# Kernel tuning notes

Hardware: AMD Instinct MI355X
Metric: run time of the kernel (lower is better)

Reference implementation:

```python
import jax, jax.numpy as jnp
import numpy as np

LN_EPS = 1e-5
LEAKY_SLOPE = 0.2


def setup_inputs() -> dict:
    key = jax.random.key(0)
    k = jax.random.split(key, 6)
    B, N, D, H, hd = 32768, 4, 256, 4, 64
    out_dim = H * hd
    # Weights stored as (in_dim, out_dim) so projection is h @ W (same math as torch Linear with W.T)
    return {
        "h": jax.random.normal(k[0], (B, N, D), dtype=jnp.float32),
        "edge_bias": jax.random.normal(k[1], (N, N), dtype=jnp.float32),
        "W_l": jax.random.normal(k[2], (D, out_dim), dtype=jnp.float32) * (1.0 / np.sqrt(D)),
        "W_r": jax.random.normal(k[3], (D, out_dim), dtype=jnp.float32) * (1.0 / np.sqrt(D)),
        "a": jax.random.normal(k[4], (H, hd), dtype=jnp.float32) * (1.0 / np.sqrt(hd)),
        "ln_gamma": jnp.ones((out_dim,), dtype=jnp.float32),
        "ln_beta": jnp.zeros((out_dim,), dtype=jnp.float32),
    }


def reference(h, edge_bias, W_l, W_r, a, ln_gamma, ln_beta):
    B, N, _ = h.shape
    H, d = a.shape
    g_l = (h @ W_l).reshape(B, N, H, d)
    g_r = (h @ W_r).reshape(B, N, H, d)
    # GATv2 dynamic attention: LeakyReLU applied BEFORE scoring with a
    pairwise = jax.nn.leaky_relu(g_l[:, :, None] + g_r[:, None, :], LEAKY_SLOPE)  # (B,N,N,H,d)
    e = jnp.einsum('bijhd,hd->bijh', pairwise, a)  # (B,N,N,H)
    e = e + edge_bias[None, :, :, None]
    alpha = jax.nn.softmax(e, axis=2)  # softmax over neighbor j
    # dropout is identity in eval mode
    h_prime = jnp.einsum('bijh,bjhd->bihd', alpha, g_r).reshape(B, N, H * d)
    # LayerNorm over last dim
    mu = jnp.mean(h_prime, axis=-1, keepdims=True)
    var = jnp.var(h_prime, axis=-1, keepdims=True)
    out = (h_prime - mu) * jax.lax.rsqrt(var + LN_EPS) * ln_gamma + ln_beta
    return out
```

## Files before the change

### kernel.cpp

```cpp
#include <hip/hip_runtime.h>
#include <hip/hip_bf16.h>

typedef short bf16x8 __attribute__((ext_vector_type(8)));
typedef float f32x4 __attribute__((ext_vector_type(4)));

#define LN_EPS 1e-5f
#define SLOPE 0.2f

__device__ __forceinline__ unsigned short f2bf(float f){
  __hip_bfloat16 b = __float2bfloat16(f);
  return *reinterpret_cast<unsigned short*>(&b);
}

__global__ void wconv_kernel(const float* __restrict__ Wl,
                             const float* __restrict__ Wr,
                             unsigned short* __restrict__ wbf){
  int idx = blockIdx.x * 256 + threadIdx.x;
  int c = idx & 511;
  int gg = (idx >> 9) & 3;
  int s = idx >> 11;
  int k0 = s * 32 + gg * 8;
  const float* src = (c < 256) ? (Wl + c) : (Wr + (c - 256));
  bf16x8 v;
  #pragma unroll
  for (int j = 0; j < 8; ++j) v[j] = (short)f2bf(src[(k0 + j) * 256]);
  *(bf16x8*)&wbf[(size_t)idx * 8] = v;
}

template<bool USE_WS>
__global__ __launch_bounds__(256, 2)
void gat_fused(const float* __restrict__ hin, const float* __restrict__ ebias,
               const float* __restrict__ Wl, const float* __restrict__ Wr,
               const float* __restrict__ avec, const float* __restrict__ gmw,
               const float* __restrict__ btw, const unsigned short* __restrict__ wbf,
               float* __restrict__ out){
  __shared__ __align__(16) unsigned short uni[8192];
  __shared__ float red1[128], red2[128];
  __shared__ float eb_s[16];

  const int t = threadIdx.x;
  const int lane = t & 63;
  const int w = t >> 6;
  const int b0 = blockIdx.x * 8;
  const int g = lane >> 4;
  const int ln = lane & 15;

  float av[4];
  #pragma unroll
  for (int c = 0; c < 4; ++c) av[c] = avec[w * 64 + c * 16 + ln];
  if (t < 16) eb_s[t] = ebias[t];

  {
    const float* hb = hin + (size_t)b0 * 1024;
    #pragma unroll
    for (int it = 0; it < 4; ++it){
      int q = it * 256 + t;
      int row = q >> 5;
      int c = q & 31;
      const float* src = hb + row * 256 + c * 8;
      float4 f0 = *(const float4*)src;
      float4 f1 = *(const float4*)(src + 4);
      bf16x8 v;
      v[0]=(short)f2bf(f0.x); v[1]=(short)f2bf(f0.y); v[2]=(short)f2bf(f0.z); v[3]=(short)f2bf(f0.w);
      v[4]=(short)f2bf(f1.x); v[5]=(short)f2bf(f1.y); v[6]=(short)f2bf(f1.z); v[7]=(short)f2bf(f1.w);
      *(bf16x8*)&uni[row * 256 + ((c ^ (row & 7)) << 3)] = v;
    }
  }
  __syncthreads();

  f32x4 acc[2][8];
  #pragma unroll
  for (int m = 0; m < 2; ++m)
    #pragma unroll
    for (int c = 0; c < 8; ++c)
      acc[m][c] = (f32x4){0.f, 0.f, 0.f, 0.f};

  for (int step = 0; step < 8; ++step){
    bf16x8 af[2], bfr[8];
    #pragma unroll
    for (int m = 0; m < 2; ++m){
      int row = m * 16 + ln;
      int chunk = step * 4 + g;
      af[m] = *(const bf16x8*)&uni[row * 256 + ((chunk ^ (row & 7)) << 3)];
    }
    if constexpr (USE_WS){
      const unsigned short* wp = wbf + (size_t)step * 16384 + (size_t)g * 4096
                               + (size_t)(w * 64 + ln) * 8;
      #pragma unroll
      for (int c = 0; c < 4; ++c){
        bfr[c]     = *(const bf16x8*)(wp + c * 128);
        bfr[c + 4] = *(const bf16x8*)(wp + 2048 + c * 128);
      }
    } else {
      #pragma unroll
      for (int c = 0; c < 4; ++c){
        int col = w * 64 + c * 16 + ln;
        #pragma unroll
        for (int j = 0; j < 8; ++j){
          bfr[c][j]     = (short)f2bf(Wl[(step * 32 + g * 8 + j) * 256 + col]);
          bfr[c + 4][j] = (short)f2bf(Wr[(step * 32 + g * 8 + j) * 256 + col]);
        }
      }
    }
    __builtin_amdgcn_s_setprio(1);
    #pragma unroll
    for (int m = 0; m < 2; ++m)
      #pragma unroll
      for (int c = 0; c < 8; ++c)
        acc[m][c] = __builtin_amdgcn_mfma_f32_16x16x32_bf16(af[m], bfr[c], acc[m][c], 0, 0, 0);
    __builtin_amdgcn_s_setprio(0);
  }

  #pragma unroll
  for (int m = 0; m < 2; ++m){
    float e[16];
    #pragma unroll
    for (int q = 0; q < 16; ++q) e[q] = 0.f;
    #pragma unroll
    for (int c = 0; c < 4; ++c){
      f32x4 GL = acc[m][c];
      f32x4 GR = acc[m][c + 4];
      #pragma unroll
      for (int i = 0; i < 4; ++i)
        #pragma unroll
        for (int j = 0; j < 4; ++j){
          float x = GL[i] + GR[j];
          x = fmaxf(x, SLOPE * x);
          e[i * 4 + j] = fmaf(x, av[c], e[i * 4 + j]);
        }
    }
    #pragma unroll
    for (int mask = 1; mask <= 8; mask <<= 1)
      #pragma unroll
      for (int q = 0; q < 16; ++q)
        e[q] += __shfl_xor(e[q], mask);
    #pragma unroll
    for (int q = 0; q < 16; ++q) e[q] += eb_s[q];
    #pragma unroll
    for (int i = 0; i < 4; ++i){
      float mx = fmaxf(fmaxf(e[i*4+0], e[i*4+1]), fmaxf(e[i*4+2], e[i*4+3]));
      float p0 = __expf(e[i*4+0] - mx);
      float p1 = __expf(e[i*4+1] - mx);
      float p2 = __expf(e[i*4+2] - mx);
      float p3 = __expf(e[i*4+3] - mx);
      float rs = 1.f / (p0 + p1 + p2 + p3);
      e[i*4+0] = p0 * rs; e[i*4+1] = p1 * rs; e[i*4+2] = p2 * rs; e[i*4+3] = p3 * rs;
    }
    float hp[4][4];
    #pragma unroll
    for (int i = 0; i < 4; ++i){
      #pragma unroll
      for (int c = 0; c < 4; ++c){
        f32x4 GR = acc[m][c + 4];
        float v = e[i*4+0] * GR[0];
        v = fmaf(e[i*4+1], GR[1], v);
        v = fmaf(e[i*4+2], GR[2], v);
        v = fmaf(e[i*4+3], GR[3], v);
        hp[i][c] = v;
      }
      float s1 = hp[i][0] + hp[i][1] + hp[i][2] + hp[i][3];
      float s2 = fmaf(hp[i][0], hp[i][0],
                 fmaf(hp[i][1], hp[i][1],
                 fmaf(hp[i][2], hp[i][2], hp[i][3] * hp[i][3])));
      #pragma unroll
      for (int mask = 1; mask <= 8; mask <<= 1){
        s1 += __shfl_xor(s1, mask);
        s2 += __shfl_xor(s2, mask);
      }
      int r = (m * 4 + g) * 4 + i;
      if (ln == 0){ red1[r * 4 + w] = s1; red2[r * 4 + w] = s2; }
    }
    __syncthreads();

    float gmr[4], btr[4];
    #pragma unroll
    for (int c = 0; c < 4; ++c){
      gmr[c] = gmw[w * 64 + c * 16 + ln];
      btr[c] = btw[w * 64 + c * 16 + ln];
    }
    #pragma unroll
    for (int i = 0; i < 4; ++i){
      int r = (m * 4 + g) * 4 + i;
      float4 v1 = *(const float4*)&red1[r * 4];
      float4 v2 = *(const float4*)&red2[r * 4];
      float s1 = (v1.x + v1.y) + (v1.z + v1.w);
      float s2 = (v2.x + v2.y) + (v2.z + v2.w);
      float mu = s1 * (1.f / 256.f);
      float var = s2 * (1.f / 256.f) - mu * mu;
      float inv = rsqrtf(var + LN_EPS);
      float* op = out + ((size_t)b0 * 4 + r) * 256 + w * 64 + ln;
      #pragma unroll
      for (int c = 0; c < 4; ++c)
        op[c * 16] = fmaf((hp[i][c] - mu) * inv, gmr[c], btr[c]);
    }
  }
}

extern "C" void kernel_launch(void* const* d_in, const int* in_sizes, int n_in,
                              void* d_out, int out_size, void* d_ws, size_t ws_size,
                              hipStream_t stream){
  const float* h  = (const float*)d_in[0];
  const float* eb = (const float*)d_in[1];
  const float* Wl = (const float*)d_in[2];
  const float* Wr = (const float*)d_in[3];
  const float* a  = (const float*)d_in[4];
  const float* gm = (const float*)d_in[5];
  const float* bt = (const float*)d_in[6];
  float* out = (float*)d_out;
  (void)n_in; (void)out_size;

  int B = in_sizes[0] / 1024;
  int nblk = B / 8;

  if (ws_size >= 262144){
    unsigned short* wbf = (unsigned short*)d_ws;
    wconv_kernel<<<64, 256, 0, stream>>>(Wl, Wr, wbf);
    gat_fused<true><<<nblk, 256, 0, stream>>>(h, eb, Wl, Wr, a, gm, bt, wbf, out);
  } else {
    gat_fused<false><<<nblk, 256, 0, stream>>>(h, eb, Wl, Wr, a, gm, bt, nullptr, out);
  }
}
```

Baseline: 97.06 us.

## Split fused GAT kernel into GEMM and attention kernels via bf16 workspace

Splits the single fused kernel into a projection GEMM kernel that writes g_l/g_r as bf16 into a workspace, and a separate attention+LayerNorm kernel that reads them back. The aim is to lower register pressure and let each phase run at better occupancy. In exchange it adds a global round trip of about 128MB of bf16 intermediates plus an extra launch, and rounds the projection outputs to bf16, which costs precision. The path is taken only when the workspace is large enough.

```diff
diff --git a/kernel.cpp b/kernel.cpp
--- a/kernel.cpp
+++ b/kernel.cpp
@@ -7,6 +7,9 @@
 #define LN_EPS 1e-5f
 #define SLOPE 0.2f
 
+__device__ __forceinline__ float bf2f(unsigned short s){
+  return __uint_as_float(((unsigned)s) << 16);
+}
 __device__ __forceinline__ unsigned short f2bf(float f){
   __hip_bfloat16 b = __float2bfloat16(f);
   return *reinterpret_cast<unsigned short*>(&b);
@@ -25,6 +28,190 @@
   #pragma unroll
   for (int j = 0; j < 8; ++j) v[j] = (short)f2bf(src[(k0 + j) * 256]);
   *(bf16x8*)&wbf[(size_t)idx * 8] = v;
+}
+
+__global__ __launch_bounds__(256, 2)
+void gemm_g(const float* __restrict__ hin, const unsigned short* __restrict__ wbf,
+            unsigned short* __restrict__ gws){
+  __shared__ __align__(16) unsigned short uni[8192];
+  const int t = threadIdx.x;
+  const int lane = t & 63;
+  const int w = t >> 6;
+  const int b0 = blockIdx.x * 8;
+  const int g = lane >> 4;
+  const int ln = lane & 15;
+
+  {
+    const float* hb = hin + (size_t)b0 * 1024;
+    #pragma unroll
+    for (int it = 0; it < 4; ++it){
+      int q = it * 256 + t;
+      int row = q >> 5;
+      int c = q & 31;
+      const float* src = hb + row * 256 + c * 8;
+      float4 f0 = *(const float4*)src;
+      float4 f1 = *(const float4*)(src + 4);
+      bf16x8 v;
+      v[0]=(short)f2bf(f0.x); v[1]=(short)f2bf(f0.y); v[2]=(short)f2bf(f0.z); v[3]=(short)f2bf(f0.w);
+      v[4]=(short)f2bf(f1.x); v[5]=(short)f2bf(f1.y); v[6]=(short)f2bf(f1.z); v[7]=(short)f2bf(f1.w);
+      *(bf16x8*)&uni[row * 256 + ((c ^ (row & 7)) << 3)] = v;
+    }
+  }
+  __syncthreads();
+
+  f32x4 acc[2][8];
+  #pragma unroll
+  for (int m = 0; m < 2; ++m)
+    #pragma unroll
+    for (int c = 0; c < 8; ++c)
+      acc[m][c] = (f32x4){0.f, 0.f, 0.f, 0.f};
+
+  for (int step = 0; step < 8; ++step){
+    bf16x8 af[2], bfr[8];
+    #pragma unroll
+    for (int m = 0; m < 2; ++m){
+      int row = m * 16 + ln;
+      int chunk = step * 4 + g;
+      af[m] = *(const bf16x8*)&uni[row * 256 + ((chunk ^ (row & 7)) << 3)];
+    }
+    const unsigned short* wp = wbf + (size_t)step * 16384 + (size_t)g * 4096
+                             + (size_t)(w * 64 + ln) * 8;
+    #pragma unroll
+    for (int c = 0; c < 4; ++c){
+      bfr[c]     = *(const bf16x8*)(wp + c * 128);
+      bfr[c + 4] = *(const bf16x8*)(wp + 2048 + c * 128);
+    }
+    __builtin_amdgcn_s_setprio(1);
+    #pragma unroll
+    for (int m = 0; m < 2; ++m)
+      #pragma unroll
+      for (int c = 0; c < 8; ++c)
+        acc[m][c] = __builtin_amdgcn_mfma_f32_16x16x32_bf16(af[m], bfr[c], acc[m][c], 0, 0, 0);
+    __builtin_amdgcn_s_setprio(0);
+  }
+
+  #pragma unroll
+  for (int m = 0; m < 2; ++m)
+    #pragma unroll
+    for (int c = 0; c < 8; ++c){
+      ushort4 s;
+      s.x = f2bf(acc[m][c][0]); s.y = f2bf(acc[m][c][1]);
+      s.z = f2bf(acc[m][c][2]); s.w = f2bf(acc[m][c][3]);
+      size_t idx16 = (((size_t)blockIdx.x * 4 + w) * 2 + m) * 8 + c;
+      *(ushort4*)&gws[idx16 * 256 + lane * 4] = s;
+    }
+}
+
+__global__ __launch_bounds__(256, 2)
+void attn_g(const unsigned short* __restrict__ gws, const float* __restrict__ ebias,
+            const float* __restrict__ avec, const float* __restrict__ gmw,
+            const float* __restrict__ btw, float* __restrict__ out){
+  __shared__ float red1[128], red2[128];
+  __shared__ float eb_s[16];
+  const int t = threadIdx.x;
+  const int lane = t & 63;
+  const int w = t >> 6;
+  const int b0 = blockIdx.x * 8;
+  const int g = lane >> 4;
+  const int ln = lane & 15;
+
+  float av[4];
+  #pragma unroll
+  for (int c = 0; c < 4; ++c) av[c] = avec[w * 64 + c * 16 + ln];
+  if (t < 16) eb_s[t] = ebias[t];
+  __syncthreads();
+
+  #pragma unroll
+  for (int m = 0; m < 2; ++m){
+    f32x4 acc[8];
+    #pragma unroll
+    for (int c = 0; c < 8; ++c){
+      size_t idx16 = (((size_t)blockIdx.x * 4 + w) * 2 + m) * 8 + c;
+      ushort4 s = *(const ushort4*)&gws[idx16 * 256 + lane * 4];
+      acc[c] = (f32x4){bf2f(s.x), bf2f(s.y), bf2f(s.z), bf2f(s.w)};
+    }
+
+    float e[16];
+    #pragma unroll
+    for (int q = 0; q < 16; ++q) e[q] = 0.f;
+    #pragma unroll
+    for (int c = 0; c < 4; ++c){
+      f32x4 GL = acc[c];
+      f32x4 GR = acc[c + 4];
+      #pragma unroll
+      for (int i = 0; i < 4; ++i)
+        #pragma unroll
+        for (int j = 0; j < 4; ++j){
+          float x = GL[i] + GR[j];
+          x = fmaxf(x, SLOPE * x);
+          e[i * 4 + j] = fmaf(x, av[c], e[i * 4 + j]);
+        }
+    }
+    #pragma unroll
+    for (int mask = 1; mask <= 8; mask <<= 1)
+      #pragma unroll
+      for (int q = 0; q < 16; ++q)
+        e[q] += __shfl_xor(e[q], mask);
+    #pragma unroll
+    for (int q = 0; q < 16; ++q) e[q] += eb_s[q];
+    #pragma unroll
+    for (int i = 0; i < 4; ++i){
+      float mx = fmaxf(fmaxf(e[i*4+0], e[i*4+1]), fmaxf(e[i*4+2], e[i*4+3]));
+      float p0 = __expf(e[i*4+0] - mx);
+      float p1 = __expf(e[i*4+1] - mx);
+      float p2 = __expf(e[i*4+2] - mx);
+      float p3 = __expf(e[i*4+3] - mx);
+      float rs = 1.f / (p0 + p1 + p2 + p3);
+      e[i*4+0] = p0 * rs; e[i*4+1] = p1 * rs; e[i*4+2] = p2 * rs; e[i*4+3] = p3 * rs;
+    }
+    float hp[4][4];
+    #pragma unroll
+    for (int i = 0; i < 4; ++i){
+      #pragma unroll
+      for (int c = 0; c < 4; ++c){
+        f32x4 GR = acc[c + 4];
+        float v = e[i*4+0] * GR[0];
+        v = fmaf(e[i*4+1], GR[1], v);
+        v = fmaf(e[i*4+2], GR[2], v);
+        v = fmaf(e[i*4+3], GR[3], v);
+        hp[i][c] = v;
+      }
+      float s1 = hp[i][0] + hp[i][1] + hp[i][2] + hp[i][3];
+      float s2 = fmaf(hp[i][0], hp[i][0],
+                 fmaf(hp[i][1], hp[i][1],
+                 fmaf(hp[i][2], hp[i][2], hp[i][3] * hp[i][3])));
+      #pragma unroll
+      for (int mask = 1; mask <= 8; mask <<= 1){
+        s1 += __shfl_xor(s1, mask);
+        s2 += __shfl_xor(s2, mask);
+      }
+      int r = (m * 4 + g) * 4 + i;
+      if (ln == 0){ red1[r * 4 + w] = s1; red2[r * 4 + w] = s2; }
+    }
+    __syncthreads();
+
+    float gmr[4], btr[4];
+    #pragma unroll
+    for (int c = 0; c < 4; ++c){
+      gmr[c] = gmw[w * 64 + c * 16 + ln];
+      btr[c] = btw[w * 64 + c * 16 + ln];
+    }
+    #pragma unroll
+    for (int i = 0; i < 4; ++i){
+      int r = (m * 4 + g) * 4 + i;
+      float4 v1 = *(const float4*)&red1[r * 4];
+      float4 v2 = *(const float4*)&red2[r * 4];
+      float s1 = (v1.x + v1.y) + (v1.z + v1.w);
+      float s2 = (v2.x + v2.y) + (v2.z + v2.w);
+      float mu = s1 * (1.f / 256.f);
+      float var = s2 * (1.f / 256.f) - mu * mu;
+      float inv = rsqrtf(var + LN_EPS);
+      float* op = out + ((size_t)b0 * 4 + r) * 256 + w * 64 + ln;
+      #pragma unroll
+      for (int c = 0; c < 4; ++c)
+        op[c * 16] = fmaf((hp[i][c] - mu) * inv, gmr[c], btr[c]);
+    }
+  }
 }
 
 template<bool USE_WS>
@@ -211,8 +398,15 @@
 
   int B = in_sizes[0] / 1024;
   int nblk = B / 8;
-
-  if (ws_size >= 262144){
+  size_t gbytes = (size_t)B * 4 * 512 * 2;
+
+  if (ws_size >= 262144 + gbytes){
+    unsigned short* wbf = (unsigned short*)d_ws;
+    unsigned short* gws = wbf + 131072;
+    wconv_kernel<<<64, 256, 0, stream>>>(Wl, Wr, wbf);
+    gemm_g<<<nblk, 256, 0, stream>>>(h, wbf, gws);
+    attn_g<<<nblk, 256, 0, stream>>>(gws, eb, a, gm, bt, out);
+  } else if (ws_size >= 262144){
     unsigned short* wbf = (unsigned short*)d_ws;
     wconv_kernel<<<64, 256, 0, stream>>>(Wl, Wr, wbf);
     gat_fused<true><<<nblk, 256, 0, stream>>>(h, eb, Wl, Wr, a, gm, bt, wbf, out);
```

Result: slower. 142.3 us (+46.6%).
